# Performance work log

Measured on AMD Instinct MI355X. Metric: run time of the kernel, lower is better.

Reference implementation:

```python
import jax, jax.numpy as jnp
import numpy as np

N = 50000      # nodes
E = 800000     # edges (avg degree 16)
LM = 1024      # lm_dim
H = 128        # hidden_channels
OUT = 64       # out_channels


def setup_inputs() -> dict:
    key = jax.random.key(0)
    ks = jax.random.split(key, 13)
    s = 0.02
    return {
        "x": jax.random.normal(ks[0], (N,), dtype=jnp.float32),
        "x_out": jax.random.normal(ks[1], (N, LM), dtype=jnp.float32),
        "c": jax.random.normal(ks[2], (N,), dtype=jnp.float32),
        "edge_index": jax.random.randint(ks[3], (2, E), 0, N, dtype=jnp.int64),
        "edge_weight": jax.random.uniform(ks[4], (E,), dtype=jnp.float32),
        # weights stored as [in, out]
        "Wa": jax.random.normal(ks[5], (1, LM), dtype=jnp.float32) * s,   # aa_linear (no bias)
        "Wc": jax.random.normal(ks[6], (1, LM), dtype=jnp.float32) * s,   # c_linear (no bias)
        "Wl": jax.random.normal(ks[7], (LM, LM), dtype=jnp.float32) * s,  # lm_linear
        "bl": jax.random.normal(ks[8], (LM,), dtype=jnp.float32) * s,
        "W1": jax.random.normal(ks[9], (LM, H), dtype=jnp.float32) * s,   # conv1
        "b1": jax.random.normal(ks[10], (H,), dtype=jnp.float32) * s,
        "W3": jax.random.normal(ks[11], (H, OUT), dtype=jnp.float32) * s,  # conv3
        "b3": jax.random.normal(ks[12], (OUT,), dtype=jnp.float32) * s,
    }


def gcn_conv(h, src, dst, ew, W, b, n):
    """PyG GCNConv with normalize=True, add_self_loops=True."""
    h = h @ W                                   # [n, out]
    loop = jnp.arange(n, dtype=src.dtype)
    src_f = jnp.concatenate([src, loop])
    dst_f = jnp.concatenate([dst, loop])
    ew_f = jnp.concatenate([ew, jnp.ones((n,), ew.dtype)])
    deg = jax.ops.segment_sum(ew_f, dst_f, num_segments=n)     # in-degree incl. self-loops
    dis = jnp.where(deg > 0, jax.lax.rsqrt(deg), 0.0)          # deg^{-1/2}
    norm = dis[src_f] * ew_f * dis[dst_f]                      # per-edge coefficient
    out = jax.ops.segment_sum(norm[:, None] * h[src_f], dst_f, num_segments=n)
    return out + b


def reference(x, x_out, c, edge_index, edge_weight, Wa, Wc, Wl, bl, W1, b1, W3, b3):
    # (c_linear(c[:,None]) + aa_linear(x[:,None]) + lm_linear(x_out)).relu()
    h = jax.nn.relu(c[:, None] * Wc[0] + x[:, None] * Wa[0] + x_out @ Wl + bl)  # [N, LM]
    src, dst = edge_index[0], edge_index[1]
    h = jax.nn.relu(gcn_conv(h, src, dst, edge_weight, W1, b1, N))              # [N, H]
    return gcn_conv(h, src, dst, edge_weight, W3, b3, N)                        # [N, OUT]
```

## Files before the change

kernel.cpp:

```cpp
#include <hip/hip_runtime.h>
#include <hip/hip_bf16.h>

typedef unsigned short u16;
typedef unsigned long long u64;
typedef __attribute__((ext_vector_type(8))) short bf16x8;
typedef __attribute__((ext_vector_type(4))) float f32x4;

constexpr int NN = 50000;
constexpr int NE = 800000;
constexpr int LM = 1024;
constexpr int HC = 128;
constexpr int OC = 64;

constexpr size_t OFF_ROWPTR = 0;
constexpr size_t OFF_CURSOR = 200192;
constexpr size_t OFF_PK     = 400384;
constexpr size_t OFF_INCL   = 800512;
constexpr size_t OFF_BSUM   = 1000704;
constexpr size_t OFF_DIS    = 1000960;
constexpr size_t OFF_META   = 1201152;
constexpr size_t OFF_WLT    = 7601408;
constexpr size_t OFF_W1T    = 9698560;
constexpr size_t OFF_H      = 9960704;
constexpr size_t OFF_Y1     = 112360704;
constexpr size_t OFF_Y3     = 125160704;
constexpr size_t OFF_ABF    = 131560704;
constexpr size_t NEED_FAST  = OFF_ABF + (size_t)NN * LM * 2;

__device__ __forceinline__ u16 f2bf(float f) {
    union { float f; unsigned int u; } a; a.f = f;
    unsigned int u = a.u + 0x7FFFu + ((a.u >> 16) & 1u);
    return (u16)(u >> 16);
}
__device__ __forceinline__ float bf2f(u16 v) {
    union { unsigned int u; float f; } a; a.u = ((unsigned int)v) << 16;
    return a.f;
}
__device__ __forceinline__ ushort2 pkbf(float a, float b) {
    union { __hip_bfloat162 h; ushort2 u; } cv;
    cv.h = __float22bfloat162_rn(make_float2(a, b));
    return cv.u;
}
__device__ __forceinline__ void async_copy16(u16* lds, const u16* g) {
    __builtin_amdgcn_global_load_lds(
        (const __attribute__((address_space(1))) void*)g,
        (__attribute__((address_space(3))) void*)lds, 16, 0, 0);
}

__global__ void k_setup(u64* __restrict__ pk,
                        const float* __restrict__ Wl, u16* __restrict__ WlT,
                        const float* __restrict__ W1, u16* __restrict__ W1T) {
    int b = blockIdx.x, t = threadIdx.x;
    if (b < 196) {
        int i = b * 256 + t;
        if (i < NN) pk[i] = 0ULL;
    } else if (b < 196 + 1024) {
        __shared__ float sm[32][33];
        int bb = b - 196;
        int n0 = (bb & 31) * 32, k0 = (bb >> 5) * 32;
        int ty = t >> 5, tx = t & 31;
        #pragma unroll
        for (int i = 0; i < 4; i++)
            sm[ty + i * 8][tx] = Wl[(size_t)(k0 + ty + i * 8) * LM + n0 + tx];
        __syncthreads();
        #pragma unroll
        for (int i = 0; i < 4; i++)
            WlT[(size_t)(n0 + ty + i * 8) * LM + k0 + tx] = f2bf(sm[tx][ty + i * 8]);
    } else {
        int idx = (b - 1220) * 256 + t;
        if (idx < HC * LM) {
            int o = idx >> 10, k = idx & 1023;
            W1T[idx] = f2bf(W1[(size_t)k * HC + o]);
        }
    }
}

__global__ void k_count(const int* __restrict__ ei, const float* __restrict__ ew,
                        u64* __restrict__ pk) {
    int e = blockIdx.x * 256 + threadIdx.x;
    if (e < NE) {
        int d = ei[NE + e];
        u64 add = (1ULL << 48) | (u64)(ew[e] * 4294967296.0);
        atomicAdd(&pk[d], add);
    }
}
__global__ void k_scan1(const u64* __restrict__ pk, int* __restrict__ incl,
                        int* __restrict__ bsum) {
    __shared__ int sm[1024];
    int t = threadIdx.x, idx = blockIdx.x * 1024 + t;
    int v = (idx < NN) ? (int)(pk[idx] >> 48) : 0;
    sm[t] = v; __syncthreads();
    for (int off = 1; off < 1024; off <<= 1) {
        int add = (t >= off) ? sm[t - off] : 0;
        __syncthreads();
        sm[t] += add;
        __syncthreads();
    }
    if (idx < NN) incl[idx] = sm[t];
    if (t == 1023) bsum[blockIdx.x] = sm[t];
}
__global__ void k_scan3(const int* __restrict__ incl, const u64* __restrict__ pk,
                        const int* __restrict__ bsum,
                        int* __restrict__ rowptr, int* __restrict__ cursor,
                        float* __restrict__ dis) {
    int seg = blockIdx.x >> 2;
    int lane = threadIdx.x & 63;
    int v = (lane < seg) ? bsum[lane] : 0;
    #pragma unroll
    for (int off = 32; off > 0; off >>= 1) v += __shfl_down(v, off, 64);
    int boffv = __shfl(v, 0, 64);
    int idx = blockIdx.x * 256 + threadIdx.x;
    if (idx < NN) {
        u64 p = pk[idx];
        int cnt = (int)(p >> 48);
        float deg = (float)((double)(p & 0xFFFFFFFFFFFFULL) * 2.3283064365386963e-10);
        int rp = incl[idx] - cnt + boffv;
        rowptr[idx] = rp;
        cursor[idx] = rp;
        dis[idx] = rsqrtf(1.0f + deg);
    } else if (idx == NN) {
        rowptr[NN] = NE;
    }
}
__global__ void k_fill(const int* __restrict__ ei, const float* __restrict__ ew,
                       const float* __restrict__ dis,
                       int* __restrict__ cursor, int2* __restrict__ meta) {
    int e = blockIdx.x * 256 + threadIdx.x;
    if (e < NE) {
        int s = ei[e];
        int d = ei[NE + e];
        int slot = atomicAdd(&cursor[d], 1);
        meta[slot] = make_int2(s, __float_as_int(ew[e] * dis[s]));
    }
}

__global__ __launch_bounds__(256) void k_cvtA(const float* __restrict__ A32,
                                              u16* __restrict__ Abf) {
    size_t idx = (size_t)blockIdx.x * 256 + threadIdx.x;
    const float* src = A32 + idx * 8;
    float4 v0 = *(const float4*)(src);
    float4 v1 = *(const float4*)(src + 4);
    union { ushort2 u2[4]; bf16x8 v; } pk;
    pk.u2[0] = pkbf(v0.x, v0.y);
    pk.u2[1] = pkbf(v0.z, v0.w);
    pk.u2[2] = pkbf(v1.x, v1.y);
    pk.u2[3] = pkbf(v1.z, v1.w);
    *(bf16x8*)(Abf + idx * 8) = pk.v;
}

constexpr int BKD = 32;
constexpr int NTK = LM / BKD;
constexpr int BUFW = (128 + 256) * BKD;

__global__ __launch_bounds__(512, 2) void k_gemm1b(
    const u16* __restrict__ Abf, const u16* __restrict__ Bt, u16* __restrict__ Cout,
    const float* __restrict__ xv, const float* __restrict__ cv,
    const float* __restrict__ Wa, const float* __restrict__ Wc,
    const float* __restrict__ bl) {
    __shared__ u16 lds[4][BUFW];
    const int tid = threadIdx.x;
    const int lane = tid & 63, wv = tid >> 6;
    const int fr = lane & 15, qd = lane >> 4;
    int wgid = (blockIdx.x & 7) * 196 + (blockIdx.x >> 3);
    const int bx = wgid >> 2, by = wgid & 3;
    const int m0 = bx * 128, n0 = by * 256;
    const int wm = (wv >> 2) * 64, wn = (wv & 3) * 64;
    const int sk = (qd ^ ((fr >> 1) & 3)) * 8;

    const int srow = lane >> 2;
    const int sslot = lane & 3;

    f32x4 acc[4][4] = {};

    auto stageA = [&](int ks, int st) {
        int rl = wv * 16 + srow;
        int row = m0 + rl; if (row >= NN) row = NN - 1;
        int k8 = sslot ^ ((rl >> 1) & 3);
        const u16* g = Abf + (size_t)row * LM + ks * BKD + k8 * 8;
        async_copy16(&lds[st][(wv * 16) * BKD], g);
    };
    auto stageB = [&](int ks, int st) {
        #pragma unroll
        for (int i = 0; i < 2; i++) {
            int r0 = wv * 32 + i * 16;
            int rl = r0 + srow;
            int k8 = sslot ^ ((rl >> 1) & 3);
            const u16* g = Bt + (size_t)(n0 + rl) * LM + ks * BKD + k8 * 8;
            async_copy16(&lds[st][128 * BKD + r0 * BKD], g);
        }
    };

    stageA(0, 0); stageB(0, 0);
    stageA(1, 1); stageB(1, 1);
    stageA(2, 2); stageB(2, 2);
    asm volatile("s_waitcnt vmcnt(6)" ::: "memory");
    __builtin_amdgcn_s_barrier();
    asm volatile("" ::: "memory");

    for (int t = 0; t < NTK; t++) {
        const u16* bA = &lds[t & 3][0];
        const u16* bB = &lds[t & 3][128 * BKD];
        bf16x8 af[4], bf[4];
        #pragma unroll
        for (int mi = 0; mi < 4; mi++)
            af[mi] = *(const bf16x8*)&bA[(wm + mi * 16 + fr) * BKD + sk];
        #pragma unroll
        for (int ni = 0; ni < 4; ni++)
            bf[ni] = *(const bf16x8*)&bB[(wn + ni * 16 + fr) * BKD + sk];
        int ks = (t + 3 < NTK) ? t + 3 : NTK - 1;
        int st = (t + 3) & 3;
        stageA(ks, st);
        stageB(ks, st);
        asm volatile("s_waitcnt vmcnt(6)" ::: "memory");
        __builtin_amdgcn_s_barrier();
        asm volatile("" ::: "memory");
        __builtin_amdgcn_s_setprio(1);
        #pragma unroll
        for (int mi = 0; mi < 4; mi++)
            #pragma unroll
            for (int ni = 0; ni < 4; ni++)
                acc[mi][ni] = __builtin_amdgcn_mfma_f32_16x16x32_bf16(
                    af[mi], bf[ni], acc[mi][ni], 0, 0, 0);
        __builtin_amdgcn_s_setprio(0);
        asm volatile("" ::: "memory");
        __builtin_amdgcn_s_barrier();
        asm volatile("" ::: "memory");
    }

    asm volatile("s_waitcnt vmcnt(0)" ::: "memory");

    int jj[4]; float waj[4], wcj[4], blj[4];
    #pragma unroll
    for (int ni = 0; ni < 4; ni++) {
        jj[ni] = n0 + wn + ni * 16 + fr;
        waj[ni] = Wa[jj[ni]]; wcj[ni] = Wc[jj[ni]]; blj[ni] = bl[jj[ni]];
    }
    #pragma unroll
    for (int mi = 0; mi < 4; mi++)
        #pragma unroll
        for (int r = 0; r < 4; r++) {
            int row = m0 + wm + mi * 16 + qd * 4 + r;
            if (row < NN) {
                float xb = xv[row], cb = cv[row];
                #pragma unroll
                for (int ni = 0; ni < 4; ni++) {
                    float v = acc[mi][ni][r] + xb * waj[ni] + cb * wcj[ni] + blj[ni];
                    Cout[(size_t)row * LM + jj[ni]] = f2bf(fmaxf(v, 0.f));
                }
            }
        }
}

__global__ __launch_bounds__(256, 2) void k_gemm1f(
    const float* __restrict__ A32, const u16* __restrict__ Bt, u16* __restrict__ Cout,
    const float* __restrict__ xv, const float* __restrict__ cv,
    const float* __restrict__ Wa, const float* __restrict__ Wc,
    const float* __restrict__ bl) {
    __shared__ u16 lA[128 * 64];
    __shared__ u16 lB[2][128 * 64];
    const int tid = threadIdx.x;
    const int lane = tid & 63, wv = tid >> 6;
    const int bx = ((blockIdx.x >> 5) << 3) | (blockIdx.x & 7);
    const int by = (blockIdx.x >> 3) & 3;
    if (bx >= 391) return;
    const int m0 = bx * 128, n0 = by * 256;
    const int wm = (wv >> 1) * 64, wn = (wv & 1) * 64;
    const int fr = lane & 15, qd = lane >> 4;

    f32x4 acc[2][4][4] = {};

    int srl[4], sslot[4]; const float* sbase[4];
    float4 pf[8];
    #pragma unroll
    for (int i = 0; i < 4; i++) {
        int cidx = i * 256 + tid;
        srl[i] = cidx >> 3; sslot[i] = cidx & 7;
        int k8 = sslot[i] ^ (srl[i] & 7);
        int row = m0 + srl[i]; if (row >= NN) row = NN - 1;
        sbase[i] = A32 + (size_t)row * LM + k8 * 8;
    }
    #pragma unroll
    for (int i = 0; i < 4; i++) {
        pf[2 * i]     = *(const float4*)(sbase[i]);
        pf[2 * i + 1] = *(const float4*)(sbase[i] + 4);
    }

    for (int kt = 0; kt < 16; kt++) {
        const int k0 = kt << 6;
        __syncthreads();
        #pragma unroll
        for (int h = 0; h < 2; h++)
            #pragma unroll
            for (int i = 0; i < 4; i++) {
                int r0 = i * 32 + wv * 8;
                int rl = r0 + (lane >> 3);
                int slot = lane & 7;
                int k8 = slot ^ (rl & 7);
                const u16* g = Bt + (size_t)(n0 + h * 128 + rl) * LM + k0 + k8 * 8;
                async_copy16(&lB[h][r0 * 64], g);
            }
        #pragma unroll
        for (int i = 0; i < 4; i++) {
            union { ushort2 u2[4]; bf16x8 v; } pk;
            pk.u2[0] = pkbf(pf[2 * i].x, pf[2 * i].y);
            pk.u2[1] = pkbf(pf[2 * i].z, pf[2 * i].w);
            pk.u2[2] = pkbf(pf[2 * i + 1].x, pf[2 * i + 1].y);
            pk.u2[3] = pkbf(pf[2 * i + 1].z, pf[2 * i + 1].w);
            *(bf16x8*)&lA[srl[i] * 64 + sslot[i] * 8] = pk.v;
        }
        __syncthreads();
        if (kt < 15) {
            #pragma unroll
            for (int i = 0; i < 4; i++) {
                pf[2 * i]     = *(const float4*)(sbase[i] + k0 + 64);
                pf[2 * i + 1] = *(const float4*)(sbase[i] + k0 + 68);
            }
        }
        #pragma unroll
        for (int s = 0; s < 2; s++) {
            const int slot = (s * 4 + qd) ^ (fr & 7);
            bf16x8 af[4];
            #pragma unroll
            for (int mi = 0; mi < 4; mi++)
                af[mi] = *(const bf16x8*)&lA[(wm + mi * 16 + fr) * 64 + slot * 8];
            #pragma unroll
            for (int h = 0; h < 2; h++) {
                bf16x8 bfm[4];
                #pragma unroll
                for (int ni = 0; ni < 4; ni++)
                    bfm[ni] = *(const bf16x8*)&lB[h][(wn + ni * 16 + fr) * 64 + slot * 8];
                #pragma unroll
                for (int mi = 0; mi < 4; mi++)
                    #pragma unroll
                    for (int ni = 0; ni < 4; ni++)
                        acc[h][mi][ni] = __builtin_amdgcn_mfma_f32_16x16x32_bf16(
                            af[mi], bfm[ni], acc[h][mi][ni], 0, 0, 0);
            }
        }
    }

    #pragma unroll
    for (int h = 0; h < 2; h++) {
        int jj[4]; float waj[4], wcj[4], blj[4];
        #pragma unroll
        for (int ni = 0; ni < 4; ni++) {
            jj[ni] = n0 + h * 128 + wn + ni * 16 + fr;
            waj[ni] = Wa[jj[ni]]; wcj[ni] = Wc[jj[ni]]; blj[ni] = bl[jj[ni]];
        }
        #pragma unroll
        for (int mi = 0; mi < 4; mi++)
            #pragma unroll
            for (int r = 0; r < 4; r++) {
                int row = m0 + wm + mi * 16 + qd * 4 + r;
                if (row < NN) {
                    float xb = xv[row], cb = cv[row];
                    #pragma unroll
                    for (int ni = 0; ni < 4; ni++) {
                        float v = acc[h][mi][ni][r] + xb * waj[ni] + cb * wcj[ni] + blj[ni];
                        Cout[(size_t)row * LM + jj[ni]] = f2bf(fmaxf(v, 0.f));
                    }
                }
            }
    }
}

__global__ __launch_bounds__(256) void k_gemm2(
    const u16* __restrict__ Abf, const u16* __restrict__ Bt, u16* __restrict__ Cout) {
    __shared__ u16 lA[64 * 64];
    __shared__ u16 lB[128 * 64];
    const int tid = threadIdx.x;
    const int lane = tid & 63, wv = tid >> 6;
    const int m0 = blockIdx.x * 64;
    const int wm = (wv >> 1) * 32, wn = (wv & 1) * 64;
    const int fr = lane & 15, qd = lane >> 4;
    f32x4 acc[2][4] = {};

    for (int kt = 0; kt < 16; kt++) {
        const int k0 = kt << 6;
        __syncthreads();
        #pragma unroll
        for (int i = 0; i < 4; i++) {
            int r0 = i * 32 + wv * 8;
            int rl = r0 + (lane >> 3);
            int slot = lane & 7;
            int k8 = slot ^ (rl & 7);
            const u16* g = Bt + (size_t)rl * LM + k0 + k8 * 8;
            async_copy16(&lB[r0 * 64], g);
        }
        #pragma unroll
        for (int i = 0; i < 2; i++) {
            int r0 = i * 32 + wv * 8;
            int rl = r0 + (lane >> 3);
            int slot = lane & 7;
            int k8 = slot ^ (rl & 7);
            int row = m0 + rl; if (row >= NN) row = NN - 1;
            const u16* g = Abf + (size_t)row * LM + k0 + k8 * 8;
            async_copy16(&lA[r0 * 64], g);
        }
        __syncthreads();
        #pragma unroll
        for (int s = 0; s < 2; s++) {
            const int slot = (s * 4 + qd) ^ (fr & 7);
            bf16x8 af[2], bfm[4];
            #pragma unroll
            for (int mi = 0; mi < 2; mi++)
                af[mi] = *(const bf16x8*)&lA[(wm + mi * 16 + fr) * 64 + slot * 8];
            #pragma unroll
            for (int ni = 0; ni < 4; ni++)
                bfm[ni] = *(const bf16x8*)&lB[(wn + ni * 16 + fr) * 64 + slot * 8];
            #pragma unroll
            for (int mi = 0; mi < 2; mi++)
                #pragma unroll
                for (int ni = 0; ni < 4; ni++)
                    acc[mi][ni] = __builtin_amdgcn_mfma_f32_16x16x32_bf16(
                        af[mi], bfm[ni], acc[mi][ni], 0, 0, 0);
        }
    }
    #pragma unroll
    for (int mi = 0; mi < 2; mi++)
        #pragma unroll
        for (int r = 0; r < 4; r++) {
            int row = m0 + wm + mi * 16 + qd * 4 + r;
            if (row < NN) {
                #pragma unroll
                for (int ni = 0; ni < 4; ni++)
                    Cout[(size_t)row * HC + wn + ni * 16 + fr] = f2bf(acc[mi][ni][r]);
            }
        }
}

__global__ __launch_bounds__(512) void k_agg1g3(
    const u16* __restrict__ y1, const int* __restrict__ rowptr,
    const int2* __restrict__ meta, const float* __restrict__ dis,
    const float* __restrict__ b1, const float* __restrict__ W3,
    u16* __restrict__ y3) {
    __shared__ float hrow[8][HC];
    int wv = threadIdx.x >> 6, lane = threadIdx.x & 63;
    int node = blockIdx.x * 8 + wv;
    if (node >= NN) return;
    float di = dis[node];
    int p0 = rowptr[node], p1 = rowptr[node + 1];
    ushort2 sv = *(const ushort2*)(y1 + (size_t)node * HC + lane * 2);
    float a0 = di * bf2f(sv.x), a1 = di * bf2f(sv.y);
    #pragma unroll 8
    for (int p = p0; p < p1; ++p) {
        int2 m = meta[p];
        float nm = __int_as_float(m.y);
        ushort2 v = *(const ushort2*)(y1 + (size_t)m.x * HC + lane * 2);
        a0 += nm * bf2f(v.x);
        a1 += nm * bf2f(v.y);
    }
    a0 = fmaxf(di * a0 + b1[lane * 2], 0.f);
    a1 = fmaxf(di * a1 + b1[lane * 2 + 1], 0.f);
    hrow[wv][lane * 2] = a0;
    hrow[wv][lane * 2 + 1] = a1;
    float acc = 0.f;
    #pragma unroll 8
    for (int k = 0; k < HC; ++k)
        acc += hrow[wv][k] * W3[(size_t)k * OC + lane];
    y3[(size_t)node * OC + lane] = f2bf(acc);
}

__global__ __launch_bounds__(256) void k_agg3(
    const u16* __restrict__ y3, const int* __restrict__ rowptr,
    const int2* __restrict__ meta, const float* __restrict__ dis,
    const float* __restrict__ b3, float* __restrict__ outp) {
    int node = blockIdx.x * 4 + (threadIdx.x >> 6);
    int lane = threadIdx.x & 63;
    if (node >= NN) return;
    float di = dis[node];
    int p0 = rowptr[node], p1 = rowptr[node + 1];
    float a = di * bf2f(y3[(size_t)node * OC + lane]);
    #pragma unroll 8
    for (int p = p0; p < p1; ++p) {
        int2 m = meta[p];
        a += __int_as_float(m.y) * bf2f(y3[(size_t)m.x * OC + lane]);
    }
    outp[(size_t)node * OC + lane] = di * a + b3[lane];
}

extern "C" void kernel_launch(void* const* d_in, const int* in_sizes, int n_in,
                              void* d_out, int out_size, void* d_ws, size_t ws_size,
                              hipStream_t stream) {
    const float* x    = (const float*)d_in[0];
    const float* xout = (const float*)d_in[1];
    const float* c    = (const float*)d_in[2];
    const int*   ei   = (const int*)d_in[3];
    const float* ew   = (const float*)d_in[4];
    const float* Wa   = (const float*)d_in[5];
    const float* Wc   = (const float*)d_in[6];
    const float* Wl   = (const float*)d_in[7];
    const float* bl   = (const float*)d_in[8];
    const float* W1   = (const float*)d_in[9];
    const float* b1   = (const float*)d_in[10];
    const float* W3   = (const float*)d_in[11];
    const float* b3   = (const float*)d_in[12];
    float* outp = (float*)d_out;

    char* ws = (char*)d_ws;
    int*   rowptr = (int*)(ws + OFF_ROWPTR);
    int*   cursor = (int*)(ws + OFF_CURSOR);
    u64*   pk     = (u64*)(ws + OFF_PK);
    int*   incl   = (int*)(ws + OFF_INCL);
    int*   bsum   = (int*)(ws + OFF_BSUM);
    float* dis    = (float*)(ws + OFF_DIS);
    int2*  meta   = (int2*)(ws + OFF_META);
    u16*   WlT    = (u16*)(ws + OFF_WLT);
    u16*   W1T    = (u16*)(ws + OFF_W1T);
    u16*   hbuf   = (u16*)(ws + OFF_H);
    u16*   y1     = (u16*)(ws + OFF_Y1);
    u16*   y3     = (u16*)(ws + OFF_Y3);
    u16*   Abf    = (u16*)(ws + OFF_ABF);

    k_setup<<<1732, 256, 0, stream>>>(pk, Wl, WlT, W1, W1T);
    k_count<<<3125, 256, 0, stream>>>(ei, ew, pk);
    k_scan1<<<49, 1024, 0, stream>>>(pk, incl, bsum);
    k_scan3<<<196, 256, 0, stream>>>(incl, pk, bsum, rowptr, cursor, dis);
    k_fill <<<3125, 256, 0, stream>>>(ei, ew, dis, cursor, meta);

    if (ws_size >= NEED_FAST) {
        k_cvtA  <<<25000, 256, 0, stream>>>(xout, Abf);
        k_gemm1b<<<392 * 4, 512, 0, stream>>>(Abf, WlT, hbuf, x, c, Wa, Wc, bl);
    } else {
        k_gemm1f<<<49 * 32, 256, 0, stream>>>(xout, WlT, hbuf, x, c, Wa, Wc, bl);
    }
    k_gemm2<<<782, 256, 0, stream>>>(hbuf, W1T, y1);
    k_agg1g3<<<6250, 512, 0, stream>>>(y1, rowptr, meta, dis, b1, W3, y3);
    k_agg3<<<12500, 256, 0, stream>>>(y3, rowptr, meta, dis, b3, outp);
}
```

Measured before the change: 735.3 us.

## Rewrite main GEMM with 256x256 tiles and 8-phase interleaved async pipeline

Replaces the 128x256 tile, BK=32, 4-stage GEMM with a 256x256 tile, BK=64 double-buffered kernel. Each K step is split into eight sub-phases, and each phase issues one half-tile async load while doing the MFMAs for one quadrant. The larger tile halves redundant global loads of the weight matrix and raises arithmetic intensity per LDS byte. In exchange it doubles the accumulator registers (32 f32x4 per thread), uses 128KB of LDS, and launches only 784 workgroups, which may hurt occupancy and load balance.

```diff
diff --git a/kernel.cpp b/kernel.cpp
--- a/kernel.cpp
+++ b/kernel.cpp
@@ -148,104 +148,133 @@
     *(bf16x8*)(Abf + idx * 8) = pk.v;
 }
 
-constexpr int BKD = 32;
-constexpr int NTK = LM / BKD;
-constexpr int BUFW = (128 + 256) * BKD;
-
-__global__ __launch_bounds__(512, 2) void k_gemm1b(
+__global__ __launch_bounds__(512, 2) void k_gemm1c(
     const u16* __restrict__ Abf, const u16* __restrict__ Bt, u16* __restrict__ Cout,
     const float* __restrict__ xv, const float* __restrict__ cv,
     const float* __restrict__ Wa, const float* __restrict__ Wc,
     const float* __restrict__ bl) {
-    __shared__ u16 lds[4][BUFW];
+    __shared__ u16 lsA[2][256 * 64];
+    __shared__ u16 lsB[2][256 * 64];
     const int tid = threadIdx.x;
     const int lane = tid & 63, wv = tid >> 6;
     const int fr = lane & 15, qd = lane >> 4;
-    int wgid = (blockIdx.x & 7) * 196 + (blockIdx.x >> 3);
+    const int fx = fr & 7;
+    const int wr16 = (wv >> 2) * 16, wc16 = (wv & 3) * 16;
+    int wgid = (blockIdx.x & 7) * 98 + (blockIdx.x >> 3);
     const int bx = wgid >> 2, by = wgid & 3;
-    const int m0 = bx * 128, n0 = by * 256;
-    const int wm = (wv >> 2) * 64, wn = (wv & 3) * 64;
-    const int sk = (qd ^ ((fr >> 1) & 3)) * 8;
-
-    const int srow = lane >> 2;
-    const int sslot = lane & 3;
-
-    f32x4 acc[4][4] = {};
-
-    auto stageA = [&](int ks, int st) {
-        int rl = wv * 16 + srow;
-        int row = m0 + rl; if (row >= NN) row = NN - 1;
-        int k8 = sslot ^ ((rl >> 1) & 3);
-        const u16* g = Abf + (size_t)row * LM + ks * BKD + k8 * 8;
-        async_copy16(&lds[st][(wv * 16) * BKD], g);
+    const int m0 = bx * 256, n0 = by * 256;
+
+    const int rl0 = tid >> 3;
+    const int k8 = (tid & 7) ^ (rl0 & 7);
+    const u16* pA[2][2];
+    #pragma unroll
+    for (int half = 0; half < 2; half++)
+        #pragma unroll
+        for (int j = 0; j < 2; j++) {
+            int row = m0 + half * 128 + j * 64 + rl0;
+            if (row >= NN) row = NN - 1;
+            pA[half][j] = Abf + (size_t)row * LM + k8 * 8;
+        }
+    const u16* pB0 = Bt + (size_t)(n0 + rl0) * LM + k8 * 8;
+
+    f32x4 acc[8][4] = {};
+
+    auto stA = [&](int kt, int half, int b) {
+        #pragma unroll
+        for (int j = 0; j < 2; j++)
+            async_copy16(&lsA[b][(half * 128 + j * 64 + wv * 8) * 64],
+                         pA[half][j] + kt * 64);
     };
-    auto stageB = [&](int ks, int st) {
-        #pragma unroll
-        for (int i = 0; i < 2; i++) {
-            int r0 = wv * 32 + i * 16;
-            int rl = r0 + srow;
-            int k8 = sslot ^ ((rl >> 1) & 3);
-            const u16* g = Bt + (size_t)(n0 + rl) * LM + ks * BKD + k8 * 8;
-            async_copy16(&lds[st][128 * BKD + r0 * BKD], g);
-        }
+    auto stB = [&](int kt, int half, int b) {
+        #pragma unroll
+        for (int j = 0; j < 2; j++)
+            async_copy16(&lsB[b][(half * 128 + j * 64 + wv * 8) * 64],
+                         pB0 + (size_t)(half * 128 + j * 64) * LM + kt * 64);
     };
 
-    stageA(0, 0); stageB(0, 0);
-    stageA(1, 1); stageB(1, 1);
-    stageA(2, 2); stageB(2, 2);
-    asm volatile("s_waitcnt vmcnt(6)" ::: "memory");
+    auto gphase = [&](auto BUF, auto MH, auto NH, auto VM, auto&& stage) {
+        constexpr int b = decltype(BUF)::value;
+        constexpr int mh = decltype(MH)::value;
+        constexpr int nh = decltype(NH)::value;
+        bf16x8 af[4][2], bq[2][2];
+        #pragma unroll
+        for (int f4 = 0; f4 < 4; f4++) {
+            int rowA = (mh * 4 + f4) * 32 + wr16 + fr;
+            #pragma unroll
+            for (int kk = 0; kk < 2; kk++)
+                af[f4][kk] = *(const bf16x8*)&lsA[b][rowA * 64 + ((kk * 4 + qd) ^ fx) * 8];
+        }
+        #pragma unroll
+        for (int n2 = 0; n2 < 2; n2++) {
+            int rowB = (nh * 2 + n2) * 64 + wc16 + fr;
+            #pragma unroll
+            for (int kk = 0; kk < 2; kk++)
+                bq[n2][kk] = *(const bf16x8*)&lsB[b][rowB * 64 + ((kk * 4 + qd) ^ fx) * 8];
+        }
+        stage();
+        asm volatile("" ::: "memory");
+        __builtin_amdgcn_s_barrier();
+        asm volatile("s_waitcnt lgkmcnt(0)" ::: "memory");
+        __builtin_amdgcn_sched_barrier(0);
+        __builtin_amdgcn_s_setprio(1);
+        #pragma unroll
+        for (int kk = 0; kk < 2; kk++)
+            #pragma unroll
+            for (int f4 = 0; f4 < 4; f4++)
+                #pragma unroll
+                for (int n2 = 0; n2 < 2; n2++)
+                    acc[mh * 4 + f4][nh * 2 + n2] = __builtin_amdgcn_mfma_f32_16x16x32_bf16(
+                        af[f4][kk], bq[n2][kk], acc[mh * 4 + f4][nh * 2 + n2], 0, 0, 0);
+        __builtin_amdgcn_s_setprio(0);
+        asm volatile("" ::: "memory");
+        if constexpr (decltype(VM)::value) {
+            asm volatile("s_waitcnt vmcnt(4)" ::: "memory");
+        }
+        __builtin_amdgcn_s_barrier();
+        asm volatile("" ::: "memory");
+    };
+    using c0 = std::integral_constant<int, 0>;
+    using c1 = std::integral_constant<int, 1>;
+    using bf_ = std::integral_constant<bool, false>;
+    using bt_ = std::integral_constant<bool, true>;
+
+    stA(0, 0, 0); stB(0, 0, 0); stA(0, 1, 0); stB(0, 1, 0);
+    stA(1, 0, 1); stB(1, 0, 1);
+    asm volatile("s_waitcnt vmcnt(4)" ::: "memory");
     __builtin_amdgcn_s_barrier();
     asm volatile("" ::: "memory");
 
-    for (int t = 0; t < NTK; t++) {
-        const u16* bA = &lds[t & 3][0];
-        const u16* bB = &lds[t & 3][128 * BKD];
-        bf16x8 af[4], bf[4];
-        #pragma unroll
-        for (int mi = 0; mi < 4; mi++)
-            af[mi] = *(const bf16x8*)&bA[(wm + mi * 16 + fr) * BKD + sk];
-        #pragma unroll
-        for (int ni = 0; ni < 4; ni++)
-            bf[ni] = *(const bf16x8*)&bB[(wn + ni * 16 + fr) * BKD + sk];
-        int ks = (t + 3 < NTK) ? t + 3 : NTK - 1;
-        int st = (t + 3) & 3;
-        stageA(ks, st);
-        stageB(ks, st);
-        asm volatile("s_waitcnt vmcnt(6)" ::: "memory");
-        __builtin_amdgcn_s_barrier();
-        asm volatile("" ::: "memory");
-        __builtin_amdgcn_s_setprio(1);
-        #pragma unroll
-        for (int mi = 0; mi < 4; mi++)
-            #pragma unroll
-            for (int ni = 0; ni < 4; ni++)
-                acc[mi][ni] = __builtin_amdgcn_mfma_f32_16x16x32_bf16(
-                    af[mi], bf[ni], acc[mi][ni], 0, 0, 0);
-        __builtin_amdgcn_s_setprio(0);
-        asm volatile("" ::: "memory");
-        __builtin_amdgcn_s_barrier();
-        asm volatile("" ::: "memory");
-    }
-
+    for (int i = 0; i < 8; ++i) {
+        const int E = 2 * i;
+        const bool g = (i < 7);
+        gphase(c0{}, c0{}, c0{}, bf_{}, [&] { stA(E + 1, 1, 1); });
+        gphase(c0{}, c0{}, c1{}, bf_{}, [&] { stB(E + 1, 1, 1); });
+        gphase(c0{}, c1{}, c0{}, bf_{}, [&] { if (g) stA(E + 2, 0, 0); });
+        gphase(c0{}, c1{}, c1{}, bt_{}, [&] { if (g) stB(E + 2, 0, 0); });
+        gphase(c1{}, c0{}, c0{}, bf_{}, [&] { if (g) stA(E + 2, 1, 0); });
+        gphase(c1{}, c0{}, c1{}, bf_{}, [&] { if (g) stB(E + 2, 1, 0); });
+        gphase(c1{}, c1{}, c0{}, bf_{}, [&] { if (g) stA(E + 3, 0, 1); });
+        gphase(c1{}, c1{}, c1{}, bt_{}, [&] { if (g) stB(E + 3, 0, 1); });
+    }
     asm volatile("s_waitcnt vmcnt(0)" ::: "memory");
 
     int jj[4]; float waj[4], wcj[4], blj[4];
     #pragma unroll
-    for (int ni = 0; ni < 4; ni++) {
-        jj[ni] = n0 + wn + ni * 16 + fr;
-        waj[ni] = Wa[jj[ni]]; wcj[ni] = Wc[jj[ni]]; blj[ni] = bl[jj[ni]];
-    }
-    #pragma unroll
-    for (int mi = 0; mi < 4; mi++)
+    for (int n = 0; n < 4; n++) {
+        jj[n] = n0 + n * 64 + wc16 + fr;
+        waj[n] = Wa[jj[n]]; wcj[n] = Wc[jj[n]]; blj[n] = bl[jj[n]];
+    }
+    #pragma unroll
+    for (int f = 0; f < 8; f++)
         #pragma unroll
         for (int r = 0; r < 4; r++) {
-            int row = m0 + wm + mi * 16 + qd * 4 + r;
+            int row = m0 + f * 32 + wr16 + qd * 4 + r;
             if (row < NN) {
                 float xb = xv[row], cb = cv[row];
                 #pragma unroll
-                for (int ni = 0; ni < 4; ni++) {
-                    float v = acc[mi][ni][r] + xb * waj[ni] + cb * wcj[ni] + blj[ni];
-                    Cout[(size_t)row * LM + jj[ni]] = f2bf(fmaxf(v, 0.f));
+                for (int n = 0; n < 4; n++) {
+                    float v = acc[f][n][r] + xb * waj[n] + cb * wcj[n] + blj[n];
+                    Cout[(size_t)row * LM + jj[n]] = f2bf(fmaxf(v, 0.f));
                 }
             }
         }
@@ -520,7 +549,7 @@
 
     if (ws_size >= NEED_FAST) {
         k_cvtA  <<<25000, 256, 0, stream>>>(xout, Abf);
-        k_gemm1b<<<392 * 4, 512, 0, stream>>>(Abf, WlT, hbuf, x, c, Wa, Wc, bl);
+        k_gemm1c<<<784, 512, 0, stream>>>(Abf, WlT, hbuf, x, c, Wa, Wc, bl);
     } else {
         k_gemm1f<<<49 * 32, 256, 0, stream>>>(xout, WlT, hbuf, x, c, Wa, Wc, bl);
     }
```

Measured after the change: 749.3 us. About the same (+1.9%).
